# Performance work log

Hardware: AMD Instinct MI355X
Metric: run time of the kernel (lower is better)

Reference implementation:

```python
import jax, jax.numpy as jnp
import numpy as np

B, T, C = 2, 1024, 1024
H, D = 16, 64
E, I = 16, 256
EPS = 1e-5


def _ln(x, g, b):
    mu = x.mean(-1, keepdims=True)
    var = ((x - mu) ** 2).mean(-1, keepdims=True)
    return (x - mu) * jax.lax.rsqrt(var + EPS) * g + b


def setup_inputs() -> dict:
    key = jax.random.key(0)
    ks = jax.random.split(key, 10)
    s = 0.02
    return {
        "hidden_states": jax.random.normal(ks[0], (B, T, C), jnp.float32),
        "ln1_g": jnp.ones((C,), jnp.float32), "ln1_b": jnp.zeros((C,), jnp.float32),
        "ln2_g": jnp.ones((C,), jnp.float32), "ln2_b": jnp.zeros((C,), jnp.float32),
        "wq": jax.random.normal(ks[1], (C, C), jnp.float32) * s,
        "wk": jax.random.normal(ks[2], (C, C), jnp.float32) * s,
        "wv": jax.random.normal(ks[3], (C, C), jnp.float32) * s,
        "wo": jax.random.normal(ks[4], (C, C), jnp.float32) * s,
        "sim_matrix": jax.random.normal(ks[5], (C, E), jnp.float32),
        "threshold": jnp.zeros((1,), jnp.float32),
        "w1": jax.random.normal(ks[6], (E, C, I), jnp.float32) * s,
        "w2": jax.random.normal(ks[7], (E, I, C), jnp.float32) * s,
    }


def reference(hidden_states, ln1_g, ln1_b, ln2_g, ln2_b, wq, wk, wv, wo,
              sim_matrix, threshold, w1, w2):
    x = hidden_states
    # ---- attention (causal SDPA) ----
    h = _ln(x, ln1_g, ln1_b)
    q = (h @ wq).reshape(B, T, H, D)
    k = (h @ wk).reshape(B, T, H, D)
    v = (h @ wv).reshape(B, T, H, D)
    logits = jnp.einsum('bqhd,bkhd->bhqk', q, k) / np.float32(np.sqrt(D))
    causal = jnp.tril(jnp.ones((T, T), bool))
    logits = jnp.where(causal, logits, jnp.float32(-1e9))
    attn = jax.nn.softmax(logits, axis=-1)
    ao = jnp.einsum('bhqk,bkhd->bqhd', attn, v).reshape(B, T, C) @ wo
    x = x + ao
    # ---- MoE ----
    h2 = _ln(x, ln2_g, ln2_b).reshape(-1, C)          # [N, C]
    xn = h2 / jnp.linalg.norm(h2, axis=-1, keepdims=True)
    wn = sim_matrix / jnp.linalg.norm(sim_matrix, axis=0, keepdims=True)
    scores = xn @ wn                                   # [N, E]
    mask = scores > threshold                          # bool [N, E]
    k_per_token = mask.sum(-1)
    # dense expert compute; zero out non-activated slots (matches index_put buffer)
    mid = jax.nn.gelu(jnp.einsum('nc,eci->nei', h2, w1), approximate=False)
    expert_outputs_full = jnp.einsum('nei,eic->nec', mid, w2) * mask[:, :, None].astype(jnp.float32)
    # STE gate: value == mask, gradient flows to scores as identity
    ste = scores + jax.lax.stop_gradient(mask.astype(jnp.float32) - scores)
    final = (expert_outputs_full * ste[:, :, None]).sum(1).reshape(B, T, C)
    x = x + final
    return (x, scores, expert_outputs_full, k_per_token)
```

## Files before the change

kernel.cpp:

```cpp
#include <hip/hip_runtime.h>
#include <hip/hip_bf16.h>
#include <math.h>

#define BB 2
#define TT 1024
#define CC 1024
#define HH 16
#define DD 64
#define EE 16
#define II 256
#define NN (BB*TT)
#define EPSLN 1e-5f
#define LDA 72

typedef __attribute__((ext_vector_type(8))) short short8;
typedef __attribute__((ext_vector_type(4))) short s16x4;
typedef __attribute__((ext_vector_type(4))) float f32x4;

__device__ inline void splitbf(float x, short& hi, short& lo) {
    __hip_bfloat16 h = __float2bfloat16(x);
    float hf = __bfloat162float(h);
    __hip_bfloat16 l = __float2bfloat16(x - hf);
    hi = *(short*)&h;
    lo = *(short*)&l;
}

__global__ __launch_bounds__(256) void ln_kernel(const float* __restrict__ x,
                                                 const float* __restrict__ g,
                                                 const float* __restrict__ bta,
                                                 __hip_bfloat16* __restrict__ outh,
                                                 __hip_bfloat16* __restrict__ outl) {
    const int row = blockIdx.x, tid = threadIdx.x;
    __shared__ float r1[256], r2[256];
    const float* xr = x + (long)row * CC;
    float4 xv = ((const float4*)xr)[tid];
    float s  = xv.x + xv.y + xv.z + xv.w;
    float q2 = xv.x*xv.x + xv.y*xv.y + xv.z*xv.z + xv.w*xv.w;
    r1[tid] = s; r2[tid] = q2; __syncthreads();
    for (int st = 128; st > 0; st >>= 1) {
        if (tid < st) { r1[tid] += r1[tid+st]; r2[tid] += r2[tid+st]; }
        __syncthreads();
    }
    const float mu  = r1[0] * (1.f/CC);
    const float var = r2[0] * (1.f/CC) - mu*mu;
    const float rs  = rsqrtf(var + EPSLN);
    float4 gv = ((const float4*)g)[tid];
    float4 bv = ((const float4*)bta)[tid];
    float xs[4];
    xs[0] = (xv.x-mu)*rs*gv.x + bv.x;
    xs[1] = (xv.y-mu)*rs*gv.y + bv.y;
    xs[2] = (xv.z-mu)*rs*gv.z + bv.z;
    xs[3] = (xv.w-mu)*rs*gv.w + bv.w;
    s16x4 hv, lv;
    #pragma unroll
    for (int j = 0; j < 4; j++) { short h,l; splitbf(xs[j], h, l); hv[j]=h; lv[j]=l; }
    *(s16x4*)(outh + (long)row * CC + tid*4) = hv;
    *(s16x4*)(outl + (long)row * CC + tid*4) = lv;
}

__global__ __launch_bounds__(256) void ln2_router(const float* __restrict__ xio,
                                                  const float* __restrict__ g,
                                                  const float* __restrict__ bta,
                                                  const float* __restrict__ sim,
                                                  const float* __restrict__ cn,
                                                  const float* __restrict__ thr,
                                                  __hip_bfloat16* __restrict__ h2b,
                                                  float* __restrict__ scores,
                                                  float* __restrict__ kpt,
                                                  float* __restrict__ maskb) {
    const int row = blockIdx.x, tid = threadIdx.x;
    __shared__ float r1[256], r2[256];
    __shared__ float red[256*17];
    float4 xv = ((const float4*)(xio + (long)row*CC))[tid];
    float s  = xv.x + xv.y + xv.z + xv.w;
    float q2 = xv.x*xv.x + xv.y*xv.y + xv.z*xv.z + xv.w*xv.w;
    r1[tid] = s; r2[tid] = q2; __syncthreads();
    for (int st = 128; st > 0; st >>= 1) {
        if (tid < st) { r1[tid] += r1[tid+st]; r2[tid] += r2[tid+st]; }
        __syncthreads();
    }
    const float mu  = r1[0] * (1.f/CC);
    const float var = r2[0] * (1.f/CC) - mu*mu;
    const float rs  = rsqrtf(var + EPSLN);
    float4 gv = ((const float4*)g)[tid];
    float4 bv = ((const float4*)bta)[tid];
    float ovs[4];
    ovs[0] = (xv.x-mu)*rs*gv.x + bv.x;
    ovs[1] = (xv.y-mu)*rs*gv.y + bv.y;
    ovs[2] = (xv.z-mu)*rs*gv.z + bv.z;
    ovs[3] = (xv.w-mu)*rs*gv.w + bv.w;
    {
        __hip_bfloat16* p = h2b + (long)row*CC + tid*4;
        p[0] = __float2bfloat16(ovs[0]); p[1] = __float2bfloat16(ovs[1]);
        p[2] = __float2bfloat16(ovs[2]); p[3] = __float2bfloat16(ovs[3]);
    }
    float acc[17] = {};
    #pragma unroll
    for (int j = 0; j < 4; j++) {
        const float v = ovs[j];
        acc[16] += v*v;
        const float* sr = sim + (long)(tid*4 + j)*EE;
        #pragma unroll
        for (int e2 = 0; e2 < EE; e2++) acc[e2] += v*sr[e2];
    }
    #pragma unroll
    for (int e2 = 0; e2 < 17; e2++) red[tid*17 + e2] = acc[e2];
    __syncthreads();
    for (int st = 128; st > 0; st >>= 1) {
        if (tid < st)
            for (int e2 = 0; e2 < 17; e2++) red[tid*17+e2] += red[(tid+st)*17+e2];
        __syncthreads();
    }
    if (tid < EE) {
        const float nrm = sqrtf(red[16]);
        const float sc  = red[tid] / (nrm * cn[tid]);
        scores[(long)row*EE + tid] = sc;
        const float mkv = sc > thr[0] ? 1.f : 0.f;
        maskb[(long)row*EE + tid] = mkv;
        red[tid] = mkv;
    }
    __syncthreads();
    if (tid == 0) {
        float c2 = 0.f;
        for (int e2 = 0; e2 < EE; e2++) c2 += red[e2];
        kpt[row] = c2;
    }
}

__global__ __launch_bounds__(256) void transpose_split4(const float* __restrict__ W0,
                                                        const float* __restrict__ W1,
                                                        const float* __restrict__ W2,
                                                        const float* __restrict__ W3,
                                                        __hip_bfloat16* __restrict__ Wth_base,
                                                        __hip_bfloat16* __restrict__ Wtl_base) {
    const int z = blockIdx.z;
    const float* W = (z==0) ? W0 : (z==1) ? W1 : (z==2) ? W2 : W3;
    __hip_bfloat16* Wth = Wth_base + (long)z*CC*CC;
    __hip_bfloat16* Wtl = Wtl_base + (long)z*CC*CC;
    const int n0 = blockIdx.x * 32, k0 = blockIdx.y * 32;
    __shared__ float t[32][33];
    const int tx = threadIdx.x & 31, ty = threadIdx.x >> 5;
    #pragma unroll
    for (int i = 0; i < 4; i++)
        t[ty + i*8][tx] = W[(long)(k0 + ty + i*8)*CC + n0 + tx];
    __syncthreads();
    #pragma unroll
    for (int i = 0; i < 4; i++) {
        float v = t[tx][ty + i*8];
        short h, l; splitbf(v, h, l);
        *(short*)&Wth[(long)(n0 + ty + i*8)*CC + k0 + tx] = h;
        *(short*)&Wtl[(long)(n0 + ty + i*8)*CC + k0 + tx] = l;
    }
}

__global__ __launch_bounds__(256) void transpose_f2b_both(const float* __restrict__ w1,
                                                          const float* __restrict__ w2,
                                                          __hip_bfloat16* __restrict__ w1t,
                                                          __hip_bfloat16* __restrict__ w2t) {
    const int zz = blockIdx.z;
    const int half = zz >> 4, e = zz & 15;
    const float* W; __hip_bfloat16* Wt; int K, N, nbx;
    if (half == 0) { W = w1 + (long)e*CC*II; Wt = w1t + (long)e*CC*II; K = CC; N = II; nbx = II/32; }
    else           { W = w2 + (long)e*II*CC; Wt = w2t + (long)e*II*CC; K = II; N = CC; nbx = CC/32; }
    const int bx = blockIdx.x;
    const int n0 = (bx % nbx) * 32, k0 = (bx / nbx) * 32;
    __shared__ float t[32][33];
    const int tx = threadIdx.x & 31, ty = threadIdx.x >> 5;
    #pragma unroll
    for (int i = 0; i < 4; i++)
        t[ty + i*8][tx] = W[(long)(k0 + ty + i*8)*N + n0 + tx];
    __syncthreads();
    #pragma unroll
    for (int i = 0; i < 4; i++)
        Wt[(long)(n0 + ty + i*8)*K + k0 + tx] = __float2bfloat16(t[tx][ty + i*8]);
}

__global__ __launch_bounds__(256) void transpose_v_bf16(
        const __hip_bfloat16* __restrict__ Vh, const __hip_bfloat16* __restrict__ Vl,
        __hip_bfloat16* __restrict__ Vth, __hip_bfloat16* __restrict__ Vtl) {
    const int b = blockIdx.z;
    const int c0 = blockIdx.y * 32, t0 = blockIdx.x * 32;
    __shared__ unsigned short th[32][33], tl[32][33];
    const int tx = threadIdx.x & 31, ty = threadIdx.x >> 5;
    const unsigned short* vh = (const unsigned short*)Vh;
    const unsigned short* vl = (const unsigned short*)Vl;
    #pragma unroll
    for (int i = 0; i < 4; i++) {
        const long src = ((long)b*TT + t0 + ty + i*8)*CC + c0 + tx;
        th[ty + i*8][tx] = vh[src];
        tl[ty + i*8][tx] = vl[src];
    }
    __syncthreads();
    #pragma unroll
    for (int i = 0; i < 4; i++) {
        const int gc = c0 + ty + i*8;
        const int hh = gc >> 6, d = gc & 63;
        const long dst = ((long)(b*HH + hh)*64 + d)*TT + t0 + tx;
        ((unsigned short*)Vth)[dst] = th[tx][ty + i*8];
        ((unsigned short*)Vtl)[dst] = tl[tx][ty + i*8];
    }
}

__global__ __launch_bounds__(256, 2) void gemm_split_big(
        const __hip_bfloat16* __restrict__ Ah,
        const __hip_bfloat16* __restrict__ Al,
        const __hip_bfloat16* __restrict__ Bh_base,
        const __hip_bfloat16* __restrict__ Bl_base,
        __hip_bfloat16* __restrict__ Ch_base,
        __hip_bfloat16* __restrict__ Cl_base,
        int M, int N, int K) {
    __shared__ __hip_bfloat16 Ash[128][40], Asl[128][40];
    __shared__ __hip_bfloat16 Bsh[128][40], Bsl[128][40];
    const int z = blockIdx.z;
    const __hip_bfloat16* Bth = Bh_base + (long)z * N * K;
    const __hip_bfloat16* Btl = Bl_base + (long)z * N * K;
    const int n0 = blockIdx.x * 128, m0 = blockIdx.y * 128;
    const int tid = threadIdx.x;
    const int wave = tid >> 6, lane = tid & 63;
    const int wm = (wave >> 1) * 64, wn = (wave & 1) * 64;
    const int l15 = lane & 15, quad = lane >> 4;

    f32x4 acc[4][4] = {};

    for (int k0 = 0; k0 < K; k0 += 32) {
        #pragma unroll
        for (int it = 0; it < 2; it++) {
            const int idx = tid + it*256;
            const int r = idx >> 2, kg = (idx & 3) * 8;
            *(short8*)&Ash[r][kg] = *(const short8*)(Ah + (long)(m0 + r)*K + k0 + kg);
            *(short8*)&Asl[r][kg] = *(const short8*)(Al + (long)(m0 + r)*K + k0 + kg);
            *(short8*)&Bsh[r][kg] = *(const short8*)(Bth + (long)(n0 + r)*K + k0 + kg);
            *(short8*)&Bsl[r][kg] = *(const short8*)(Btl + (long)(n0 + r)*K + k0 + kg);
        }
        __syncthreads();
        short8 ah[4], al[4], bh[4], bl[4];
        #pragma unroll
        for (int i = 0; i < 4; i++) {
            ah[i] = *(const short8*)&Ash[wm + i*16 + l15][quad*8];
            al[i] = *(const short8*)&Asl[wm + i*16 + l15][quad*8];
            bh[i] = *(const short8*)&Bsh[wn + i*16 + l15][quad*8];
            bl[i] = *(const short8*)&Bsl[wn + i*16 + l15][quad*8];
        }
        #pragma unroll
        for (int mi = 0; mi < 4; mi++)
            #pragma unroll
            for (int ni = 0; ni < 4; ni++) {
                acc[mi][ni] = __builtin_amdgcn_mfma_f32_16x16x32_bf16(ah[mi], bh[ni], acc[mi][ni], 0,0,0);
                acc[mi][ni] = __builtin_amdgcn_mfma_f32_16x16x32_bf16(ah[mi], bl[ni], acc[mi][ni], 0,0,0);
                acc[mi][ni] = __builtin_amdgcn_mfma_f32_16x16x32_bf16(al[mi], bh[ni], acc[mi][ni], 0,0,0);
            }
        __syncthreads();
    }

    #pragma unroll
    for (int mi = 0; mi < 4; mi++)
        #pragma unroll
        for (int r = 0; r < 4; r++) {
            const int row = m0 + wm + mi*16 + quad*4 + r;
            #pragma unroll
            for (int ni = 0; ni < 4; ni++) {
                const int col = n0 + wn + ni*16 + l15;
                short hh, ll; splitbf(acc[mi][ni][r], hh, ll);
                *(short*)&Ch_base[(long)z*M*N + (long)row*N + col] = hh;
                *(short*)&Cl_base[(long)z*M*N + (long)row*N + col] = ll;
            }
        }
}

__global__ __launch_bounds__(256, 2) void gemm_split(
        const __hip_bfloat16* __restrict__ Ah,
        const __hip_bfloat16* __restrict__ Al,
        const __hip_bfloat16* __restrict__ Bth,
        const __hip_bfloat16* __restrict__ Btl,
        float* __restrict__ Cp,
        int M, int N, int K,
        const float* __restrict__ resid) {
    __shared__ __hip_bfloat16 Ash[64][40], Asl[64][40];
    __shared__ __hip_bfloat16 Bsh[128][40], Bsl[128][40];
    const int n0 = blockIdx.x * 128, m0 = blockIdx.y * 64;
    const int tid = threadIdx.x;
    const int wave = tid >> 6, lane = tid & 63;
    const int wm = (wave >> 1) * 32, wn = (wave & 1) * 64;
    const int l15 = lane & 15, quad = lane >> 4;

    f32x4 acc[2][4] = {};

    for (int k0 = 0; k0 < K; k0 += 32) {
        {
            const int r = tid >> 2, kg = (tid & 3) * 8;
            *(short8*)&Ash[r][kg] = *(const short8*)(Ah + (long)(m0 + r)*K + k0 + kg);
            *(short8*)&Asl[r][kg] = *(const short8*)(Al + (long)(m0 + r)*K + k0 + kg);
        }
        #pragma unroll
        for (int it = 0; it < 2; it++) {
            const int idx = tid + it*256;
            const int r = idx >> 2, kg = (idx & 3) * 8;
            *(short8*)&Bsh[r][kg] = *(const short8*)(Bth + (long)(n0 + r)*K + k0 + kg);
            *(short8*)&Bsl[r][kg] = *(const short8*)(Btl + (long)(n0 + r)*K + k0 + kg);
        }
        __syncthreads();
        short8 ah[2], al[2], bh[4], bl[4];
        #pragma unroll
        for (int mi = 0; mi < 2; mi++) {
            ah[mi] = *(const short8*)&Ash[wm + mi*16 + l15][quad*8];
            al[mi] = *(const short8*)&Asl[wm + mi*16 + l15][quad*8];
        }
        #pragma unroll
        for (int ni = 0; ni < 4; ni++) {
            bh[ni] = *(const short8*)&Bsh[wn + ni*16 + l15][quad*8];
            bl[ni] = *(const short8*)&Bsl[wn + ni*16 + l15][quad*8];
        }
        #pragma unroll
        for (int mi = 0; mi < 2; mi++)
            #pragma unroll
            for (int ni = 0; ni < 4; ni++) {
                acc[mi][ni] = __builtin_amdgcn_mfma_f32_16x16x32_bf16(ah[mi], bh[ni], acc[mi][ni], 0,0,0);
                acc[mi][ni] = __builtin_amdgcn_mfma_f32_16x16x32_bf16(ah[mi], bl[ni], acc[mi][ni], 0,0,0);
                acc[mi][ni] = __builtin_amdgcn_mfma_f32_16x16x32_bf16(al[mi], bh[ni], acc[mi][ni], 0,0,0);
            }
        __syncthreads();
    }

    #pragma unroll
    for (int mi = 0; mi < 2; mi++)
        #pragma unroll
        for (int r = 0; r < 4; r++) {
            const int row = m0 + wm + mi*16 + quad*4 + r;
            #pragma unroll
            for (int ni = 0; ni < 4; ni++) {
                const int col = n0 + wn + ni*16 + l15;
                Cp[(long)row*N + col] = acc[mi][ni][r] + resid[(long)row*N + col];
            }
        }
}

__global__ __launch_bounds__(256) void gemm_mfma1(
        const __hip_bfloat16* __restrict__ A,
        const __hip_bfloat16* __restrict__ Bt, long sBe,
        __hip_bfloat16* __restrict__ Cp, long sCe, int ldc,
        int M, int N, int K) {
    constexpr int LDK = 40;
    __shared__ __hip_bfloat16 As[128][LDK];
    __shared__ __hip_bfloat16 Bs[128][LDK];
    const int e = blockIdx.z;
    Bt += (long)e * sBe;
    const int n0 = blockIdx.x * 128, m0 = blockIdx.y * 128;
    const int tid = threadIdx.x;
    const int wave = tid >> 6, lane = tid & 63;
    const int wm = (wave >> 1) * 64, wn = (wave & 1) * 64;
    const int l15 = lane & 15, quad = lane >> 4;

    f32x4 acc[4][4] = {};

    for (int k0 = 0; k0 < K; k0 += 32) {
        #pragma unroll
        for (int it = 0; it < 2; it++) {
            int idx = tid + it*256;
            int r = idx >> 2, kg = idx & 3;
            short8 av = *(const short8*)(A  + (long)(m0 + r)*K + k0 + kg*8);
            short8 bv = *(const short8*)(Bt + (long)(n0 + r)*K + k0 + kg*8);
            *(short8*)&As[r][kg*8] = av;
            *(short8*)&Bs[r][kg*8] = bv;
        }
        __syncthreads();
        short8 af[4], bff[4];
        #pragma unroll
        for (int i = 0; i < 4; i++) {
            af[i]  = *(const short8*)&As[wm + i*16 + l15][quad*8];
            bff[i] = *(const short8*)&Bs[wn + i*16 + l15][quad*8];
        }
        #pragma unroll
        for (int mi = 0; mi < 4; mi++)
            #pragma unroll
            for (int ni = 0; ni < 4; ni++)
                acc[mi][ni] = __builtin_amdgcn_mfma_f32_16x16x32_bf16(
                                  af[mi], bff[ni], acc[mi][ni], 0, 0, 0);
        __syncthreads();
    }

    #pragma unroll
    for (int mi = 0; mi < 4; mi++) {
        #pragma unroll
        for (int r = 0; r < 4; r++) {
            const int row = m0 + wm + mi*16 + quad*4 + r;
            #pragma unroll
            for (int ni = 0; ni < 4; ni++) {
                const int col = n0 + wn + ni*16 + l15;
                float val = acc[mi][ni][r];
                val = 0.5f*val*(1.f + erff(val*0.70710678118f));
                Cp[(long)e*sCe + (long)row*ldc + col] = __float2bfloat16(val);
            }
        }
    }
}

__global__ __launch_bounds__(256) void gemm_moe2(
        const __hip_bfloat16* __restrict__ mid,
        const __hip_bfloat16* __restrict__ w2t,
        float* __restrict__ eo,
        float* __restrict__ xio,
        const float* __restrict__ mask) {
    constexpr int LDK = 40;
    __shared__ __hip_bfloat16 As[128][LDK];
    __shared__ __hip_bfloat16 Bs[128][LDK];
    const int e0 = blockIdx.z * 4;
    const int n0 = blockIdx.x * 128, m0 = blockIdx.y * 128;
    const int tid = threadIdx.x;
    const int wave = tid >> 6, lane = tid & 63;
    const int wm = (wave >> 1) * 64, wn = (wave & 1) * 64;
    const int l15 = lane & 15, quad = lane >> 4;

    f32x4 sum[4][4] = {};

    for (int ei = 0; ei < 4; ei++) {
        const int e = e0 + ei;
        const __hip_bfloat16* A  = mid + (long)e*NN*II;
        const __hip_bfloat16* Bt = w2t + (long)e*CC*II;
        f32x4 acc[4][4] = {};
        for (int k0 = 0; k0 < II; k0 += 32) {
            #pragma unroll
            for (int it = 0; it < 2; it++) {
                int idx = tid + it*256;
                int r = idx >> 2, kg = idx & 3;
                short8 av = *(const short8*)(A  + (long)(m0 + r)*II + k0 + kg*8);
                short8 bv = *(const short8*)(Bt + (long)(n0 + r)*II + k0 + kg*8);
                *(short8*)&As[r][kg*8] = av;
                *(short8*)&Bs[r][kg*8] = bv;
            }
            __syncthreads();
            short8 af[4], bff[4];
            #pragma unroll
            for (int i = 0; i < 4; i++) {
                af[i]  = *(const short8*)&As[wm + i*16 + l15][quad*8];
                bff[i] = *(const short8*)&Bs[wn + i*16 + l15][quad*8];
            }
            #pragma unroll
            for (int mi = 0; mi < 4; mi++)
                #pragma unroll
                for (int ni = 0; ni < 4; ni++)
                    acc[mi][ni] = __builtin_amdgcn_mfma_f32_16x16x32_bf16(
                                      af[mi], bff[ni], acc[mi][ni], 0, 0, 0);
            __syncthreads();
        }
        #pragma unroll
        for (int mi = 0; mi < 4; mi++) {
            #pragma unroll
            for (int r = 0; r < 4; r++) {
                const int row = m0 + wm + mi*16 + quad*4 + r;
                const float mv = mask[(long)row*EE + e];
                #pragma unroll
                for (int ni = 0; ni < 4; ni++) {
                    const int col = n0 + wn + ni*16 + l15;
                    const float val = acc[mi][ni][r] * mv;
                    eo[((long)row*EE + e)*CC + col] = val;
                    sum[mi][ni][r] += val;
                }
            }
        }
    }

    #pragma unroll
    for (int mi = 0; mi < 4; mi++)
        #pragma unroll
        for (int r = 0; r < 4; r++) {
            const int row = m0 + wm + mi*16 + quad*4 + r;
            #pragma unroll
            for (int ni = 0; ni < 4; ni++) {
                const int col = n0 + wn + ni*16 + l15;
                atomicAdd(&xio[(long)row*CC + col], sum[mi][ni][r]);
            }
        }
}

__global__ __launch_bounds__(256, 4) void attn_split(
        const __hip_bfloat16* __restrict__ Qh, const __hip_bfloat16* __restrict__ Ql,
        const __hip_bfloat16* __restrict__ Kh, const __hip_bfloat16* __restrict__ Kl,
        const __hip_bfloat16* __restrict__ Vtg_h, const __hip_bfloat16* __restrict__ Vtg_l,
        float* __restrict__ Opart,
        float* __restrict__ mpart,
        float* __restrict__ lpart) {
    __shared__ __hip_bfloat16 KPh[64][LDA], KPl[64][LDA];
    __shared__ __hip_bfloat16 Vth[64][LDA], Vtl[64][LDA];

    const int bx = blockIdx.x;
    const int qt = 15 - (bx >> 1), half = bx & 1;
    const int h = blockIdx.y, b = blockIdx.z;
    const int tid = threadIdx.x;
    const int wave = tid >> 6, lane = tid & 63;
    const int l15 = lane & 15, quad = lane >> 4;
    const int wm = wave * 16;
    const long tbase = (long)b * TT * CC + (long)h * DD;
    const long vbase = (long)(b*HH + h) * 64 * TT;
    const int pidx = ((b*HH + h)*16 + qt)*2 + half;
    float* Op = Opart + (long)pidx * 4096;

    const int n_kt = qt + 1, mid_kt = (n_kt + 1) >> 1;
    const int kt_lo = half ? mid_kt : 0;
    const int kt_hi = half ? n_kt   : mid_kt;

    if (kt_lo >= kt_hi) {
        for (int i = tid; i < 64*64; i += 256) Op[i] = 0.f;
        if (tid < 64) { mpart[(long)pidx*64 + tid] = -1e30f; lpart[(long)pidx*64 + tid] = 0.f; }
        return;
    }

    short8 qh[2], ql[2];
    {
        const long qoff = tbase + (long)(qt*64 + wm + l15)*CC;
        #pragma unroll
        for (int kc = 0; kc < 2; kc++) {
            qh[kc] = *(const short8*)(Qh + qoff + kc*32 + quad*8);
            ql[kc] = *(const short8*)(Ql + qoff + kc*32 + quad*8);
        }
    }

    f32x4 oacc[4] = {};
    float m_run[4], l_run[4];
    #pragma unroll
    for (int r = 0; r < 4; r++) { m_run[r] = -1e30f; l_run[r] = 0.f; }

    for (int kt = kt_lo; kt < kt_hi; kt++) {
        __syncthreads();
        #pragma unroll
        for (int it = 0; it < 2; it++) {
            const int idx = tid + it*256;
            const int r = idx >> 3, g = (idx & 7)*8;
            const long koff = tbase + (long)(kt*64 + r)*CC + g;
            const long voff = vbase + (long)r*TT + kt*64 + g;
            *(short8*)&KPh[r][g] = *(const short8*)(Kh + koff);
            *(short8*)&KPl[r][g] = *(const short8*)(Kl + koff);
            *(short8*)&Vth[r][g] = *(const short8*)(Vtg_h + voff);
            *(short8*)&Vtl[r][g] = *(const short8*)(Vtg_l + voff);
        }
        __syncthreads();

        f32x4 s[4] = {};
        #pragma unroll
        for (int nt = 0; nt < 4; nt++)
            #pragma unroll
            for (int kc = 0; kc < 2; kc++) {
                short8 bh = *(const short8*)&KPh[nt*16 + l15][kc*32 + quad*8];
                short8 bl = *(const short8*)&KPl[nt*16 + l15][kc*32 + quad*8];
                s[nt] = __builtin_amdgcn_mfma_f32_16x16x32_bf16(qh[kc], bh, s[nt], 0,0,0);
                s[nt] = __builtin_amdgcn_mfma_f32_16x16x32_bf16(qh[kc], bl, s[nt], 0,0,0);
                s[nt] = __builtin_amdgcn_mfma_f32_16x16x32_bf16(ql[kc], bh, s[nt], 0,0,0);
            }

        const bool diag = (kt == qt);
        float alpha[4];
        float pr[4][4];
        #pragma unroll
        for (int r = 0; r < 4; r++) {
            const int rowg = wm + quad*4 + r;
            float sv[4], mx = -1e30f;
            #pragma unroll
            for (int nt = 0; nt < 4; nt++) {
                float val = s[nt][r] * 0.125f;
                if (diag && (nt*16 + l15) > rowg) val = -1e30f;
                sv[nt] = val;
                mx = fmaxf(mx, val);
            }
            #pragma unroll
            for (int off = 1; off < 16; off <<= 1) mx = fmaxf(mx, __shfl_xor(mx, off, 16));
            const float mnew = fmaxf(m_run[r], mx);
            alpha[r] = __expf(m_run[r] - mnew);
            float rs = 0.f;
            #pragma unroll
            for (int nt = 0; nt < 4; nt++) {
                float p = __expf(sv[nt] - mnew);
                pr[r][nt] = p;
                rs += p;
            }
            #pragma unroll
            for (int off = 1; off < 16; off <<= 1) rs += __shfl_xor(rs, off, 16);
            l_run[r] = l_run[r]*alpha[r] + rs;
            m_run[r] = mnew;
        }
        __syncthreads();

        #pragma unroll
        for (int r = 0; r < 4; r++)
            #pragma unroll
            for (int nt = 0; nt < 4; nt++) {
                short hh, ll; splitbf(pr[r][nt], hh, ll);
                *(short*)&KPh[wm + quad*4 + r][nt*16 + l15] = hh;
                *(short*)&KPl[wm + quad*4 + r][nt*16 + l15] = ll;
            }

        #pragma unroll
        for (int dt = 0; dt < 4; dt++)
            #pragma unroll
            for (int r = 0; r < 4; r++)
                oacc[dt][r] *= alpha[r];
        #pragma unroll
        for (int kc = 0; kc < 2; kc++) {
            short8 ph = *(const short8*)&KPh[wm + l15][kc*32 + quad*8];
            short8 pl = *(const short8*)&KPl[wm + l15][kc*32 + quad*8];
            #pragma unroll
            for (int dt = 0; dt < 4; dt++) {
                short8 vh = *(const short8*)&Vth[dt*16 + l15][kc*32 + quad*8];
                short8 vl = *(const short8*)&Vtl[dt*16 + l15][kc*32 + quad*8];
                oacc[dt] = __builtin_amdgcn_mfma_f32_16x16x32_bf16(ph, vh, oacc[dt], 0,0,0);
                oacc[dt] = __builtin_amdgcn_mfma_f32_16x16x32_bf16(ph, vl, oacc[dt], 0,0,0);
                oacc[dt] = __builtin_amdgcn_mfma_f32_16x16x32_bf16(pl, vh, oacc[dt], 0,0,0);
            }
        }
    }

    #pragma unroll
    for (int dt = 0; dt < 4; dt++)
        #pragma unroll
        for (int r = 0; r < 4; r++)
            Op[(wm + quad*4 + r)*64 + dt*16 + l15] = oacc[dt][r];
    if (l15 == 0) {
        #pragma unroll
        for (int r = 0; r < 4; r++) {
            mpart[(long)pidx*64 + wm + quad*4 + r] = m_run[r];
            lpart[(long)pidx*64 + wm + quad*4 + r] = l_run[r];
        }
    }
}

__global__ __launch_bounds__(256) void attn_merge(const float* __restrict__ Opart,
                                                  const float* __restrict__ mpart,
                                                  const float* __restrict__ lpart,
                                                  __hip_bfloat16* __restrict__ aoh,
                                                  __hip_bfloat16* __restrict__ aol) {
    const int qt = blockIdx.x, h = blockIdx.y, b = blockIdx.z;
    const int pA = ((b*HH + h)*16 + qt)*2, pB = pA + 1;
    const int tid = threadIdx.x;
    const int r = tid >> 2, c0 = (tid & 3) * 16;
    const float mA = mpart[(long)pA*64 + r], mB = mpart[(long)pB*64 + r];
    const float lA = lpart[(long)pA*64 + r], lB = lpart[(long)pB*64 + r];
    const float M  = fmaxf(mA, mB);
    const float wA = __expf(mA - M), wB = __expf(mB - M);
    const float inv = 1.f / (lA*wA + lB*wB);
    const float* OA = Opart + (long)pA*4096 + r*64 + c0;
    const float* OB = Opart + (long)pB*4096 + r*64 + c0;
    const long dst = (long)b*TT*CC + (long)(qt*64 + r)*CC + h*DD + c0;
    #pragma unroll
    for (int j = 0; j < 16; j += 4) {
        float4 oa = *(const float4*)(OA + j);
        float4 ob = *(const float4*)(OB + j);
        float xs[4];
        xs[0] = (oa.x*wA + ob.x*wB)*inv;
        xs[1] = (oa.y*wA + ob.y*wB)*inv;
        xs[2] = (oa.z*wA + ob.z*wB)*inv;
        xs[3] = (oa.w*wA + ob.w*wB)*inv;
        s16x4 hv, lv;
        #pragma unroll
        for (int t = 0; t < 4; t++) { short hh,ll; splitbf(xs[t],hh,ll); hv[t]=hh; lv[t]=ll; }
        *(s16x4*)(aoh + dst + j) = hv;
        *(s16x4*)(aol + dst + j) = lv;
    }
}

__global__ __launch_bounds__(256) void colnorm_kernel(const float* __restrict__ sim,
                                                      float* __restrict__ cn) {
    const int e = blockIdx.x, tid = threadIdx.x;
    __shared__ float red[256];
    float s = 0.f;
    for (int c = tid; c < CC; c += 256) {
        float vv = sim[(long)c*EE + e];
        s += vv*vv;
    }
    red[tid] = s; __syncthreads();
    for (int st = 128; st > 0; st >>= 1) {
        if (tid < st) red[tid] += red[tid+st];
        __syncthreads();
    }
    if (tid == 0) cn[e] = sqrtf(red[0]);
}

extern "C" void kernel_launch(void* const* d_in, const int* in_sizes, int n_in,
                              void* d_out, int out_size, void* d_ws, size_t ws_size,
                              hipStream_t stream) {
    const float* x     = (const float*)d_in[0];
    const float* ln1_g = (const float*)d_in[1];
    const float* ln1_b = (const float*)d_in[2];
    const float* ln2_g = (const float*)d_in[3];
    const float* ln2_b = (const float*)d_in[4];
    const float* wq    = (const float*)d_in[5];
    const float* wk    = (const float*)d_in[6];
    const float* wv    = (const float*)d_in[7];
    const float* wo    = (const float*)d_in[8];
    const float* sim   = (const float*)d_in[9];
    const float* thr   = (const float*)d_in[10];
    const float* w1    = (const float*)d_in[11];
    const float* w2    = (const float*)d_in[12];

    float* out_x      = (float*)d_out;
    float* out_scores = out_x + (long)NN*CC;
    float* out_eo     = out_scores + (long)NN*EE;
    float* out_kpt    = out_eo + (long)NN*EE*CC;

    const long MF = (long)NN*CC;
    const long CK = (long)CC*CC;
    float* ws   = (float*)d_ws;
    __hip_bfloat16* aoh = (__hip_bfloat16*)ws;
    __hip_bfloat16* aol = (__hip_bfloat16*)(ws + MF/2);
    __hip_bfloat16* qkvh = (__hip_bfloat16*)(ws + MF);
    __hip_bfloat16* qkvl = (__hip_bfloat16*)(ws + MF + 3*MF/2);
    __hip_bfloat16* vth = (__hip_bfloat16*)(ws + 4*MF);
    __hip_bfloat16* vtl = (__hip_bfloat16*)(ws + 4*MF + MF/2);
    __hip_bfloat16* h2b = (__hip_bfloat16*)(ws + 5*MF);
    float* Opart = ws + 5*MF + MF/2;
    __hip_bfloat16* hh  = (__hip_bfloat16*)(ws + 5*MF + MF/2);
    __hip_bfloat16* hl  = (__hip_bfloat16*)(ws + 6*MF);
    __hip_bfloat16* mid = (__hip_bfloat16*)(ws + 5*MF + MF/2);
    __hip_bfloat16* wsph = (__hip_bfloat16*)(ws + 7*MF + MF/2);
    __hip_bfloat16* wspl = (__hip_bfloat16*)(ws + 8*MF + MF/2);
    __hip_bfloat16* w1t  = (__hip_bfloat16*)(ws + 7*MF + MF/2);
    __hip_bfloat16* w2t  = (__hip_bfloat16*)(ws + 8*MF + MF/2);
    float* maskb = ws + 9*MF + MF/2;
    float* cn    = maskb + (long)NN*EE;
    float* mpart = cn + 16;
    float* lpart = mpart + 1024L*64;

    colnorm_kernel<<<EE, 256, 0, stream>>>(sim, cn);

    {
        dim3 gt(CC/32, CC/32, 4);
        transpose_split4<<<gt, 256, 0, stream>>>(wq, wk, wv, wo, wsph, wspl);
    }

    ln_kernel<<<NN, 256, 0, stream>>>(x, ln1_g, ln1_b, hh, hl);

    {
        dim3 gq(CC/128, NN/128, 3);
        gemm_split_big<<<gq, 256, 0, stream>>>(hh, hl, wsph, wspl,
                                               qkvh, qkvl, NN, CC, CC);
    }

    {
        dim3 gv(TT/32, CC/32, BB);
        transpose_v_bf16<<<gv, 256, 0, stream>>>(qkvh + 2*(long)NN*CC, qkvl + 2*(long)NN*CC,
                                                 vth, vtl);
    }

    {
        dim3 gattn(32, HH, BB);
        attn_split<<<gattn, 256, 0, stream>>>(qkvh, qkvl,
                                              qkvh + (long)NN*CC, qkvl + (long)NN*CC,
                                              vth, vtl, Opart, mpart, lpart);
        dim3 gmerge(16, HH, BB);
        attn_merge<<<gmerge, 256, 0, stream>>>(Opart, mpart, lpart, aoh, aol);
    }

    {
        dim3 go(CC/128, NN/64, 1);
        gemm_split<<<go, 256, 0, stream>>>(aoh, aol, wsph + 3*CK, wspl + 3*CK,
                                           out_x, NN, CC, CC, x);
    }

    {
        dim3 ge(256, 1, 2*EE);
        transpose_f2b_both<<<ge, 256, 0, stream>>>(w1, w2, w1t, w2t);
    }

    ln2_router<<<NN, 256, 0, stream>>>(out_x, ln2_g, ln2_b, sim, cn, thr,
                                       h2b, out_scores, out_kpt, maskb);

    {
        dim3 g(II/128, NN/128, EE);
        gemm_mfma1<<<g, 256, 0, stream>>>(h2b, w1t, (long)II*CC,
                                          mid, (long)NN*II, II,
                                          NN, II, CC);
    }

    {
        dim3 g(CC/128, NN/128, EE/4);
        gemm_moe2<<<g, 256, 0, stream>>>(mid, w2t, out_eo, out_x, maskb);
    }
}
```

Before: 483.7 us.

## Route tokens per expert and run sparse grouped MoE GEMMs

The router now builds per-expert token lists with atomic counters. Both expert GEMMs run only over the tokens active for each expert, gathering rows through a shared-memory row map, so MLP compute for masked-out slots is skipped. Masked slots of the expert output are zeroed by a separate kernel, and a row-wise kernel sums active expert outputs into the residual instead of using atomics. In exchange it adds two extra passes over the large expert-output tensor and makes the token order within each list depend on atomic ordering.

```diff
diff --git a/kernel.cpp b/kernel.cpp
--- a/kernel.cpp
+++ b/kernel.cpp
@@ -67,7 +67,9 @@
                                                   __hip_bfloat16* __restrict__ h2b,
                                                   float* __restrict__ scores,
                                                   float* __restrict__ kpt,
-                                                  float* __restrict__ maskb) {
+                                                  float* __restrict__ maskb,
+                                                  int* __restrict__ cnt,
+                                                  int* __restrict__ elist) {
     const int row = blockIdx.x, tid = threadIdx.x;
     __shared__ float r1[256], r2[256];
     __shared__ float red[256*17];
@@ -118,6 +120,10 @@
         const float mkv = sc > thr[0] ? 1.f : 0.f;
         maskb[(long)row*EE + tid] = mkv;
         red[tid] = mkv;
+        if (mkv > 0.f) {
+            int slot = atomicAdd(&cnt[tid], 1);
+            elist[(long)tid*NN + slot] = row;
+        }
     }
     __syncthreads();
     if (tid == 0) {
@@ -334,31 +340,39 @@
         }
 }
 
-__global__ __launch_bounds__(256) void gemm_mfma1(
+__global__ __launch_bounds__(256) void gemm_moe1_sparse(
         const __hip_bfloat16* __restrict__ A,
-        const __hip_bfloat16* __restrict__ Bt, long sBe,
-        __hip_bfloat16* __restrict__ Cp, long sCe, int ldc,
-        int M, int N, int K) {
+        const __hip_bfloat16* __restrict__ w1t,
+        __hip_bfloat16* __restrict__ mid,
+        const int* __restrict__ cnt,
+        const int* __restrict__ elist) {
     constexpr int LDK = 40;
     __shared__ __hip_bfloat16 As[128][LDK];
     __shared__ __hip_bfloat16 Bs[128][LDK];
+    __shared__ int rowmap[128];
     const int e = blockIdx.z;
-    Bt += (long)e * sBe;
-    const int n0 = blockIdx.x * 128, m0 = blockIdx.y * 128;
+    const int count = cnt[e];
+    const int m0 = blockIdx.y * 128;
+    if (m0 >= count) return;
+    const int n0 = blockIdx.x * 128;
+    const __hip_bfloat16* Bt = w1t + (long)e*II*CC;
+    const int* lst = elist + (long)e*NN;
     const int tid = threadIdx.x;
+    if (tid < 128) rowmap[tid] = lst[min(m0 + tid, count - 1)];
+    __syncthreads();
     const int wave = tid >> 6, lane = tid & 63;
     const int wm = (wave >> 1) * 64, wn = (wave & 1) * 64;
     const int l15 = lane & 15, quad = lane >> 4;
 
     f32x4 acc[4][4] = {};
 
-    for (int k0 = 0; k0 < K; k0 += 32) {
+    for (int k0 = 0; k0 < CC; k0 += 32) {
         #pragma unroll
         for (int it = 0; it < 2; it++) {
             int idx = tid + it*256;
             int r = idx >> 2, kg = idx & 3;
-            short8 av = *(const short8*)(A  + (long)(m0 + r)*K + k0 + kg*8);
-            short8 bv = *(const short8*)(Bt + (long)(n0 + r)*K + k0 + kg*8);
+            short8 av = *(const short8*)(A  + (long)rowmap[r]*CC + k0 + kg*8);
+            short8 bv = *(const short8*)(Bt + (long)(n0 + r)*CC + k0 + kg*8);
             *(short8*)&As[r][kg*8] = av;
             *(short8*)&Bs[r][kg*8] = bv;
         }
@@ -382,94 +396,116 @@
     for (int mi = 0; mi < 4; mi++) {
         #pragma unroll
         for (int r = 0; r < 4; r++) {
-            const int row = m0 + wm + mi*16 + quad*4 + r;
-            #pragma unroll
-            for (int ni = 0; ni < 4; ni++) {
-                const int col = n0 + wn + ni*16 + l15;
-                float val = acc[mi][ni][r];
-                val = 0.5f*val*(1.f + erff(val*0.70710678118f));
-                Cp[(long)e*sCe + (long)row*ldc + col] = __float2bfloat16(val);
-            }
-        }
-    }
-}
-
-__global__ __launch_bounds__(256) void gemm_moe2(
+            const int slot = m0 + wm + mi*16 + quad*4 + r;
+            if (slot < count) {
+                #pragma unroll
+                for (int ni = 0; ni < 4; ni++) {
+                    const int col = n0 + wn + ni*16 + l15;
+                    float val = acc[mi][ni][r];
+                    val = 0.5f*val*(1.f + erff(val*0.70710678118f));
+                    mid[((long)e*NN + slot)*II + col] = __float2bfloat16(val);
+                }
+            }
+        }
+    }
+}
+
+__global__ __launch_bounds__(256) void gemm_moe2_sparse(
         const __hip_bfloat16* __restrict__ mid,
         const __hip_bfloat16* __restrict__ w2t,
         float* __restrict__ eo,
-        float* __restrict__ xio,
-        const float* __restrict__ mask) {
+        const int* __restrict__ cnt,
+        const int* __restrict__ elist) {
     constexpr int LDK = 40;
     __shared__ __hip_bfloat16 As[128][LDK];
     __shared__ __hip_bfloat16 Bs[128][LDK];
-    const int e0 = blockIdx.z * 4;
-    const int n0 = blockIdx.x * 128, m0 = blockIdx.y * 128;
+    __shared__ int rowmap[128];
+    const int e = blockIdx.z;
+    const int count = cnt[e];
+    const int m0 = blockIdx.y * 128;
+    if (m0 >= count) return;
+    const int n0 = blockIdx.x * 128;
+    const __hip_bfloat16* A  = mid + (long)e*NN*II;
+    const __hip_bfloat16* Bt = w2t + (long)e*CC*II;
+    const int* lst = elist + (long)e*NN;
     const int tid = threadIdx.x;
+    if (tid < 128) rowmap[tid] = lst[min(m0 + tid, count - 1)];
+    __syncthreads();
     const int wave = tid >> 6, lane = tid & 63;
     const int wm = (wave >> 1) * 64, wn = (wave & 1) * 64;
     const int l15 = lane & 15, quad = lane >> 4;
 
-    f32x4 sum[4][4] = {};
-
-    for (int ei = 0; ei < 4; ei++) {
-        const int e = e0 + ei;
-        const __hip_bfloat16* A  = mid + (long)e*NN*II;
-        const __hip_bfloat16* Bt = w2t + (long)e*CC*II;
-        f32x4 acc[4][4] = {};
-        for (int k0 = 0; k0 < II; k0 += 32) {
-            #pragma unroll
-            for (int it = 0; it < 2; it++) {
-                int idx = tid + it*256;
-                int r = idx >> 2, kg = idx & 3;
-                short8 av = *(const short8*)(A  + (long)(m0 + r)*II + k0 + kg*8);
-                short8 bv = *(const short8*)(Bt + (long)(n0 + r)*II + k0 + kg*8);
-                *(short8*)&As[r][kg*8] = av;
-                *(short8*)&Bs[r][kg*8] = bv;
-            }
-            __syncthreads();
-            short8 af[4], bff[4];
-            #pragma unroll
-            for (int i = 0; i < 4; i++) {
-                af[i]  = *(const short8*)&As[wm + i*16 + l15][quad*8];
-                bff[i] = *(const short8*)&Bs[wn + i*16 + l15][quad*8];
-            }
-            #pragma unroll
-            for (int mi = 0; mi < 4; mi++)
-                #pragma unroll
-                for (int ni = 0; ni < 4; ni++)
-                    acc[mi][ni] = __builtin_amdgcn_mfma_f32_16x16x32_bf16(
-                                      af[mi], bff[ni], acc[mi][ni], 0, 0, 0);
-            __syncthreads();
-        }
-        #pragma unroll
-        for (int mi = 0; mi < 4; mi++) {
-            #pragma unroll
-            for (int r = 0; r < 4; r++) {
-                const int row = m0 + wm + mi*16 + quad*4 + r;
-                const float mv = mask[(long)row*EE + e];
+    f32x4 acc[4][4] = {};
+
+    for (int k0 = 0; k0 < II; k0 += 32) {
+        #pragma unroll
+        for (int it = 0; it < 2; it++) {
+            int idx = tid + it*256;
+            int r = idx >> 2, kg = idx & 3;
+            short8 av = *(const short8*)(A  + (long)(m0 + r)*II + k0 + kg*8);
+            short8 bv = *(const short8*)(Bt + (long)(n0 + r)*II + k0 + kg*8);
+            *(short8*)&As[r][kg*8] = av;
+            *(short8*)&Bs[r][kg*8] = bv;
+        }
+        __syncthreads();
+        short8 af[4], bff[4];
+        #pragma unroll
+        for (int i = 0; i < 4; i++) {
+            af[i]  = *(const short8*)&As[wm + i*16 + l15][quad*8];
+            bff[i] = *(const short8*)&Bs[wn + i*16 + l15][quad*8];
+        }
+        #pragma unroll
+        for (int mi = 0; mi < 4; mi++)
+            #pragma unroll
+            for (int ni = 0; ni < 4; ni++)
+                acc[mi][ni] = __builtin_amdgcn_mfma_f32_16x16x32_bf16(
+                                  af[mi], bff[ni], acc[mi][ni], 0, 0, 0);
+        __syncthreads();
+    }
+
+    #pragma unroll
+    for (int mi = 0; mi < 4; mi++) {
+        #pragma unroll
+        for (int r = 0; r < 4; r++) {
+            const int slot = m0 + wm + mi*16 + quad*4 + r;
+            if (slot < count) {
+                const int tok = rowmap[wm + mi*16 + quad*4 + r];
                 #pragma unroll
                 for (int ni = 0; ni < 4; ni++) {
                     const int col = n0 + wn + ni*16 + l15;
-                    const float val = acc[mi][ni][r] * mv;
-                    eo[((long)row*EE + e)*CC + col] = val;
-                    sum[mi][ni][r] += val;
+                    eo[((long)tok*EE + e)*CC + col] = acc[mi][ni][r];
                 }
             }
         }
     }
-
-    #pragma unroll
-    for (int mi = 0; mi < 4; mi++)
-        #pragma unroll
-        for (int r = 0; r < 4; r++) {
-            const int row = m0 + wm + mi*16 + quad*4 + r;
-            #pragma unroll
-            for (int ni = 0; ni < 4; ni++) {
-                const int col = n0 + wn + ni*16 + l15;
-                atomicAdd(&xio[(long)row*CC + col], sum[mi][ni][r]);
-            }
-        }
+}
+
+__global__ __launch_bounds__(256) void eo_zero(const float* __restrict__ maskb,
+                                               float* __restrict__ eo) {
+    const int row = blockIdx.x, tid = threadIdx.x;
+    const float4 z4 = {0.f, 0.f, 0.f, 0.f};
+    #pragma unroll
+    for (int e = 0; e < EE; e++) {
+        if (maskb[(long)row*EE + e] == 0.f)
+            ((float4*)(eo + ((long)row*EE + e)*CC))[tid] = z4;
+    }
+}
+
+__global__ __launch_bounds__(256) void moe_sum_masked(const float* __restrict__ maskb,
+                                                      const float* __restrict__ eo,
+                                                      float* __restrict__ xio) {
+    const int row = blockIdx.x, tid = threadIdx.x;
+    float4 s = {0.f, 0.f, 0.f, 0.f};
+    #pragma unroll
+    for (int e = 0; e < EE; e++) {
+        if (maskb[(long)row*EE + e] != 0.f) {
+            float4 v = ((const float4*)(eo + ((long)row*EE + e)*CC))[tid];
+            s.x += v.x; s.y += v.y; s.z += v.z; s.w += v.w;
+        }
+    }
+    float4 xv = ((float4*)(xio + (long)row*CC))[tid];
+    xv.x += s.x; xv.y += s.y; xv.z += s.z; xv.w += s.w;
+    ((float4*)(xio + (long)row*CC))[tid] = xv;
 }
 
 __global__ __launch_bounds__(256, 4) void attn_split(
@@ -656,7 +692,8 @@
 }
 
 __global__ __launch_bounds__(256) void colnorm_kernel(const float* __restrict__ sim,
-                                                      float* __restrict__ cn) {
+                                                      float* __restrict__ cn,
+                                                      int* __restrict__ cnt) {
     const int e = blockIdx.x, tid = threadIdx.x;
     __shared__ float red[256];
     float s = 0.f;
@@ -669,7 +706,7 @@
         if (tid < st) red[tid] += red[tid+st];
         __syncthreads();
     }
-    if (tid == 0) cn[e] = sqrtf(red[0]);
+    if (tid == 0) { cn[e] = sqrtf(red[0]); cnt[e] = 0; }
 }
 
 extern "C" void kernel_launch(void* const* d_in, const int* in_sizes, int n_in,
@@ -716,8 +753,10 @@
     float* cn    = maskb + (long)NN*EE;
     float* mpart = cn + 16;
     float* lpart = mpart + 1024L*64;
-
-    colnorm_kernel<<<EE, 256, 0, stream>>>(sim, cn);
+    int*   cnt   = (int*)(lpart + 1024L*64);
+    int*   elist = cnt + 16;
+
+    colnorm_kernel<<<EE, 256, 0, stream>>>(sim, cn, cnt);
 
     {
         dim3 gt(CC/32, CC/32, 4);
@@ -759,17 +798,20 @@
     }
 
     ln2_router<<<NN, 256, 0, stream>>>(out_x, ln2_g, ln2_b, sim, cn, thr,
-                                       h2b, out_scores, out_kpt, maskb);
+                                       h2b, out_scores, out_kpt, maskb,
+                                       cnt, elist);
+
+    eo_zero<<<NN, 256, 0, stream>>>(maskb, out_eo);
 
     {
         dim3 g(II/128, NN/128, EE);
-        gemm_mfma1<<<g, 256, 0, stream>>>(h2b, w1t, (long)II*CC,
-                                          mid, (long)NN*II, II,
-                                          NN, II, CC);
-    }
-
-    {
-        dim3 g(CC/128, NN/128, EE/4);
-        gemm_moe2<<<g, 256, 0, stream>>>(mid, w2t, out_eo, out_x, maskb);
-    }
-}
+        gemm_moe1_sparse<<<g, 256, 0, stream>>>(h2b, w1t, mid, cnt, elist);
+    }
+
+    {
+        dim3 g(CC/128, NN/128, EE);
+        gemm_moe2_sparse<<<g, 256, 0, stream>>>(mid, w2t, out_eo, cnt, elist);
+    }
+
+    moe_sum_masked<<<NN, 256, 0, stream>>>(maskb, out_eo, out_x);
+}
```

After: 470.0 us. 2.8% less time.
